# Kernel tuning notes

Hardware: AMD Instinct MI355X
Metric: run time of the kernel (lower is better)

Reference implementation:

```python
import jax, jax.numpy as jnp
import numpy as np

HEADS = 8
EMBED = 64  # out_channels per head
N_OP = 100000
N_MC = 20000
N_EDGE = 300000
EPS = 1e-16  # matches PyG softmax denominator epsilon


def hetero_gat(x_src, x_dst, edge_index, W, att, n_dst):
    """GAT conv: gather -> per-edge score -> segment softmax over dst -> scatter-sum -> head mean.
    x_src: [Ns, F], x_dst: [Nd, F], edge_index: [2, E] (row0=src, row1=dst),
    W: [HEADS*EMBED, F], att: [1, HEADS, 2*EMBED].
    """
    hs = (x_src @ W.T).reshape(-1, HEADS, EMBED)  # [Ns,H,C]
    hd = (x_dst @ W.T).reshape(-1, HEADS, EMBED)  # [Nd,H,C]
    src, dst = edge_index[0], edge_index[1]
    x_j = hs[src]                                  # [E,H,C] (source/neighbor)
    x_i = hd[dst]                                  # [E,H,C] (destination)
    att_i = att[0, :, :EMBED]                      # [H,C] weights for x_i part of concat
    att_j = att[0, :, EMBED:]                      # [H,C] weights for x_j part
    # (cat([x_i,x_j],-1) * att).sum(-1) without materializing the concat
    alpha = jnp.einsum('ehc,hc->eh', x_i, att_i) + jnp.einsum('ehc,hc->eh', x_j, att_j)
    # segment softmax grouped by destination node
    m = jax.ops.segment_max(alpha, dst, num_segments=n_dst)  # [Nd,H]
    e = jnp.exp(alpha - m[dst])
    s = jax.ops.segment_sum(e, dst, num_segments=n_dst)      # [Nd,H]
    alpha = e / (s[dst] + EPS)                                # [E,H]
    msg = x_j * alpha[..., None]                              # [E,H,C]
    out = jax.ops.segment_sum(msg, dst, num_segments=n_dst)   # [Nd,H,C]
    return out.mean(axis=1)                                   # [Nd,C] multi-head mean


def setup_inputs() -> dict:
    key = jax.random.key(0)
    ks = jax.random.split(key, 12)
    op_nodes = jax.random.normal(ks[0], (N_OP, 4), dtype=jnp.float32)
    mc_nodes = jax.random.normal(ks[1], (N_MC, 2), dtype=jnp.float32)
    src = jax.random.randint(ks[2], (N_EDGE,), 0, N_OP)
    dst = jax.random.randint(ks[3], (N_EDGE,), 0, N_MC)
    edge_index_om = jnp.stack([src, dst]).astype(jnp.int64)
    g = 0.1
    params = {
        'W_op': jax.random.normal(ks[4], (EMBED, 4), dtype=jnp.float32) * g,
        'b_op': jnp.zeros((EMBED,), dtype=jnp.float32),
        'W_mc': jax.random.normal(ks[5], (EMBED, 2), dtype=jnp.float32) * g,
        'b_mc': jnp.zeros((EMBED,), dtype=jnp.float32),
        'W_om': jax.random.normal(ks[6], (HEADS * EMBED, EMBED), dtype=jnp.float32) * g,
        'att_om': jax.random.normal(ks[7], (1, HEADS, 2 * EMBED), dtype=jnp.float32) * g,
        'W_mo': jax.random.normal(ks[8], (HEADS * EMBED, EMBED), dtype=jnp.float32) * g,
        'att_mo': jax.random.normal(ks[9], (1, HEADS, 2 * EMBED), dtype=jnp.float32) * g,
    }
    return {'op_nodes': op_nodes, 'mc_nodes': mc_nodes, 'edge_index_om': edge_index_om, **params}


def reference(op_nodes, mc_nodes, edge_index_om, W_op, b_op, W_mc, b_mc,
              W_om, att_om, W_mo, att_mo):
    h_op = jax.nn.elu(op_nodes @ W_op.T + b_op)   # [N_OP, 64]
    h_mc = jax.nn.elu(mc_nodes @ W_mc.T + b_mc)   # [N_MC, 64]
    # op -> mc
    h_mc_new = hetero_gat(h_op, h_mc, edge_index_om, W_om, att_om, N_MC)
    h_mc = jax.nn.elu(h_mc + h_mc_new)
    # mc -> op (reversed edges)
    edge_index_mo = jnp.stack([edge_index_om[1], edge_index_om[0]])
    h_op_new = hetero_gat(h_mc, h_op, edge_index_mo, W_mo, att_mo, N_OP)
    h_op = jax.nn.elu(h_op + h_op_new)
    return (h_op, h_mc)
```

## Files before the change

kernel.cpp:

```cpp
#include <hip/hip_runtime.h>
#include <hip/hip_bf16.h>

using bf16 = __hip_bfloat16;
typedef __attribute__((ext_vector_type(8))) short short8;
typedef __attribute__((ext_vector_type(4))) float f32x4;

__device__ __forceinline__ unsigned short f2bf(float f) {
  bf16 h = __float2bfloat16(f);
  return *reinterpret_cast<unsigned short*>(&h);
}
__device__ __forceinline__ float bf2f(unsigned short u) {
  return __uint_as_float(((unsigned)u) << 16);
}

__device__ __forceinline__ float loadf(const void* p, int i, int is_f32) {
  if (is_f32) return ((const float*)p)[i];
  return __bfloat162float(((const bf16*)p)[i]);
}

__global__ __launch_bounds__(256) void init_kernel(
    const int* __restrict__ ei, const unsigned short* __restrict__ x,
    int* __restrict__ flags, int* __restrict__ cnt1, int n1,
    int* __restrict__ cnt2, int n2) {
  int t = threadIdx.x;
  int g = blockIdx.x * 256 + t;
  int stride = gridDim.x * 256;
  for (int i = g; i < n1; i += stride) cnt1[i] = 0;
  for (int i = g; i < n2; i += stride) cnt2[i] = 0;
  if (blockIdx.x == 0) {
    __shared__ int red[256];
    int o = 0, big = 0;
    for (int i = t; i < 2048; i += 256) {
      o |= ei[2 * i + 1];
      float v = __uint_as_float(((unsigned)x[2 * i]) << 16);
      if (!(fabsf(v) < 1000.f)) big = 1;
    }
    red[t] = o;
    __syncthreads();
    for (int d = 128; d > 0; d >>= 1) {
      if (t < d) red[t] |= red[t + d];
      __syncthreads();
    }
    int o_all = red[0];
    __syncthreads();
    red[t] = big;
    __syncthreads();
    for (int d = 128; d > 0; d >>= 1) {
      if (t < d) red[t] |= red[t + d];
      __syncthreads();
    }
    if (t == 0) {
      flags[0] = red[0];
      flags[1] = (o_all == 0) ? 1 : 0;
    }
  }
}

__device__ __forceinline__ int edge_src(const int* ei, int E, int e, int i64) {
  return i64 ? ei[2 * e] : ei[e];
}
__device__ __forceinline__ int edge_dst(const int* ei, int E, int e, int i64) {
  return i64 ? ei[2 * E + 2 * e] : ei[E + e];
}

template <int FIN>
__device__ __forceinline__ void node_body4(
    const void* x, const void* W, const void* b, int is_f32,
    const float* vj, bf16* h_out, unsigned short* ea_out, int n0, int N) {
  int lane = threadIdx.x & 63;
  float wreg[FIN];
#pragma unroll
  for (int f = 0; f < FIN; ++f) wreg[f] = loadf(W, lane * FIN + f, is_f32);
  float bias = loadf(b, lane, is_f32);
  float vjreg[8];
  if (ea_out) {
#pragma unroll
    for (int h = 0; h < 8; ++h) vjreg[h] = vj[h * 64 + lane];
  }
#pragma unroll
  for (int j = 0; j < 4; ++j) {
    int n = n0 + j;
    if (n >= N) break;
    float acc = bias;
#pragma unroll
    for (int f = 0; f < FIN; ++f)
      acc += loadf(x, n * FIN + f, is_f32) * wreg[f];
    float hv = acc > 0.f ? acc : expm1f(acc);
    h_out[(unsigned)(n << 6) + lane] = __float2bfloat16(hv);
    if (ea_out) {
      float p[8];
#pragma unroll
      for (int h = 0; h < 8; ++h) p[h] = hv * vjreg[h];
#pragma unroll
      for (int i = 0; i < 4; ++i) {
        float send = (lane & 4) ? p[i] : p[i + 4];
        float keep = (lane & 4) ? p[i + 4] : p[i];
        p[i] = keep + __shfl_xor(send, 4, 64);
      }
#pragma unroll
      for (int i = 0; i < 2; ++i) {
        float send = (lane & 2) ? p[i] : p[i + 2];
        float keep = (lane & 2) ? p[i + 2] : p[i];
        p[i] = keep + __shfl_xor(send, 2, 64);
      }
      {
        float send = (lane & 1) ? p[0] : p[1];
        float keep = (lane & 1) ? p[1] : p[0];
        p[0] = keep + __shfl_xor(send, 1, 64);
      }
      p[0] += __shfl_xor(p[0], 8, 64);
      p[0] += __shfl_xor(p[0], 16, 64);
      p[0] += __shfl_xor(p[0], 32, 64);
      if (lane < 8) ea_out[(unsigned)(n << 3) + lane] = f2bf(__expf(p[0]));
    }
  }
}

__global__ __launch_bounds__(256) void front_kernel(
    const void* __restrict__ x_op, const void* __restrict__ W_op,
    const void* __restrict__ b_op, const void* __restrict__ x_mc,
    const void* __restrict__ W_mc, const void* __restrict__ b_mc,
    const void* __restrict__ W1, const void* __restrict__ att1,
    const void* __restrict__ W2, const void* __restrict__ att2,
    const int* __restrict__ ei, const int* __restrict__ flags,
    float* __restrict__ vj1, bf16* __restrict__ Wrt1, float* __restrict__ vj2,
    bf16* __restrict__ Wrt2, bf16* __restrict__ h_op,
    unsigned short* __restrict__ ea_op, bf16* __restrict__ h_mc,
    int* __restrict__ cnt_dst, int* __restrict__ cnt_src, int n_op, int n_mc,
    int E, int nbo, int nbm) {
  int bid = blockIdx.x;
  int is_f32 = flags[0];
  if (bid < nbo) {
    int n0 = bid * 16 + (threadIdx.x >> 6) * 4;
    if (n0 < n_op)
      node_body4<4>(x_op, W_op, b_op, is_f32, vj1, h_op, ea_op, n0, n_op);
  } else if (bid < nbo + nbm) {
    int n0 = (bid - nbo) * 16 + (threadIdx.x >> 6) * 4;
    if (n0 < n_mc)
      node_body4<2>(x_mc, W_mc, b_mc, is_f32, nullptr, h_mc, nullptr, n0, n_mc);
  } else if (bid < nbo + nbm + 256) {
    int pb = bid - nbo - nbm;
    int side = pb >= 128;
    const void* W = side ? W2 : W1;
    const void* att = side ? att2 : att1;
    float* vj = side ? vj2 : vj1;
    bf16* Wrt = side ? Wrt2 : Wrt1;
    int tt = (pb & 127) * 256 + threadIdx.x;
    if (tt < 32768) {
      int c = tt >> 9, k = tt & 511;
      int f = k >> 3, h = k & 7;
      Wrt[tt] = __float2bfloat16(loadf(W, ((h << 6) + c) * 64 + f, is_f32));
    }
    if (tt < 512) {
      int hh = tt >> 6, ff = tt & 63;
      float s = 0.f;
      for (int cc = 0; cc < 64; ++cc)
        s += loadf(att, hh * 128 + 64 + cc, is_f32) *
             loadf(W, ((hh << 6) + cc) * 64 + ff, is_f32);
      vj[tt] = s;
    }
  } else {
    int i64 = flags[1];
    int e = (bid - nbo - nbm - 256) * 256 + threadIdx.x;
    if (e < E) {
      atomicAdd(&cnt_dst[edge_dst(ei, E, e, i64)], 1);
      atomicAdd(&cnt_src[edge_src(ei, E, e, i64)], 1);
    }
  }
}

__global__ __launch_bounds__(256) void scan_bsum2(
    const int* __restrict__ cnt1, int n1, int nb1, const int* __restrict__ cnt2,
    int n2, int* __restrict__ bsum1, int* __restrict__ bsum2) {
  __shared__ int red[256];
  int t = threadIdx.x;
  int side = (int)blockIdx.x >= nb1;
  const int* cnt = side ? cnt2 : cnt1;
  int n = side ? n2 : n1;
  int blk = side ? (blockIdx.x - nb1) : blockIdx.x;
  int base = blk * 2048 + t * 8;
  int s = 0;
#pragma unroll
  for (int i = 0; i < 8; ++i)
    if (base + i < n) s += cnt[base + i];
  red[t] = s;
  __syncthreads();
  for (int d = 128; d > 0; d >>= 1) {
    if (t < d) red[t] += red[t + d];
    __syncthreads();
  }
  if (t == 0) (side ? bsum2 : bsum1)[blk] = red[0];
}

__global__ __launch_bounds__(256) void scan_write2(
    const int* __restrict__ cnt1, int n1, int nb1,
    const int* __restrict__ bsum1, int* __restrict__ offs1,
    int* __restrict__ cur1, const int* __restrict__ cnt2, int n2, int nb2,
    const int* __restrict__ bsum2, int* __restrict__ offs2,
    int* __restrict__ cur2) {
  __shared__ int red[256];
  __shared__ int base_s;
  int t = threadIdx.x;
  int side = (int)blockIdx.x >= nb1;
  const int* cnt = side ? cnt2 : cnt1;
  const int* bsum = side ? bsum2 : bsum1;
  int* offs = side ? offs2 : offs1;
  int* cur = side ? cur2 : cur1;
  int n = side ? n2 : n1;
  int nb = side ? nb2 : nb1;
  int blk = side ? (blockIdx.x - nb1) : blockIdx.x;
  if (t == 0) {
    int b = 0;
    for (int i = 0; i < blk; ++i) b += bsum[i];
    base_s = b;
  }
  int base = blk * 2048 + t * 8;
  int c[8];
  int s = 0;
#pragma unroll
  for (int i = 0; i < 8; ++i) {
    c[i] = (base + i < n) ? cnt[base + i] : 0;
    s += c[i];
  }
  red[t] = s;
  __syncthreads();
  for (int d = 1; d < 256; d <<= 1) {
    int v = red[t];
    int add = (t >= d) ? red[t - d] : 0;
    __syncthreads();
    red[t] = v + add;
    __syncthreads();
  }
  int run = base_s + red[t] - s;
#pragma unroll
  for (int i = 0; i < 8; ++i) {
    if (base + i < n) {
      offs[base + i] = run;
      cur[base + i] = run;
      run += c[i];
    }
  }
  if (blk == nb - 1 && t == 255) offs[n] = base_s + red[255];
}

__global__ __launch_bounds__(256) void fill_edges(
    const int* __restrict__ ei, int E, const int* __restrict__ flags,
    int* __restrict__ cur1, int* __restrict__ srcs1, int* __restrict__ cur2,
    int* __restrict__ srcs2) {
  int i64 = flags[1];
  int e = blockIdx.x * blockDim.x + threadIdx.x;
  if (e < E) {
    int s = edge_src(ei, E, e, i64), d = edge_dst(ei, E, e, i64);
    int p = atomicAdd(&cur1[d], 1);
    srcs1[p] = s;
    int q = atomicAdd(&cur2[s], 1);
    srcs2[q] = d;
  }
}

template <bool WRITE_AJ, bool WRITE_BF>
__global__ __launch_bounds__(256) void gat_fused(
    int Nd, const int* __restrict__ offs, const int* __restrict__ srcs,
    const unsigned short* __restrict__ ea, const bf16* __restrict__ h_src,
    const bf16* __restrict__ Wrt, const bf16* __restrict__ h_res,
    float* __restrict__ out_f32, bf16* __restrict__ out_bf,
    const float* __restrict__ vj_next, unsigned short* __restrict__ ea_next) {
  __shared__ __align__(16) unsigned short Zl[16 * 520];
  __shared__ float ajp[4][16][8];

  int t = threadIdx.x;
  int wv = t >> 6, lane = t & 63;
  int d0 = blockIdx.x * 16;
  int sj = lane >> 4;
  int fq = lane & 15;

  int dlo = d0 + wv * 4;
  int wo0 = offs[min(dlo + 0, Nd)];
  int wo1 = offs[min(dlo + 1, Nd)];
  int wo2 = offs[min(dlo + 2, Nd)];
  int wo3 = offs[min(dlo + 3, Nd)];
  int wo4 = offs[min(dlo + 4, Nd)];
  int woj = sj == 0 ? wo0 : sj == 1 ? wo1 : sj == 2 ? wo2 : wo3;
  int woj1 = sj == 0 ? wo1 : sj == 1 ? wo2 : sj == 2 ? wo3 : wo4;
  int nj = woj1 - woj;

  float z[8][4];
#pragma unroll
  for (int h = 0; h < 8; ++h)
#pragma unroll
    for (int f = 0; f < 4; ++f) z[h][f] = 0.f;
  float s8[8];
#pragma unroll
  for (int h = 0; h < 8; ++h) s8[h] = 0.f;

  const unsigned short* hsrc_u = (const unsigned short*)h_src;

  int rmax = max(nj, __shfl_xor(nj, 16, 64));
  rmax = max(rmax, __shfl_xor(rmax, 32, 64));

  for (int r0 = 0; r0 < rmax; r0 += 4) {
    unsigned srcq[4];
#pragma unroll
    for (int q = 0; q < 4; ++q) {
      int r = r0 + q;
      srcq[q] = (r < nj) ? (unsigned)srcs[woj + r] : 0u;
    }
    ushort4 uq[4];
    short8 eq[4];
#pragma unroll
    for (int q = 0; q < 4; ++q) {
      unsigned s = srcq[q];
      uq[q] = *(const ushort4*)(hsrc_u + (s << 6) + (fq << 2));
      eq[q] = *(const short8*)(ea + (s << 3));
    }
#pragma unroll
    for (int q = 0; q < 4; ++q) {
      bool act = (r0 + q) < nj;
      float w[8];
#pragma unroll
      for (int h = 0; h < 8; ++h)
        w[h] = act ? bf2f((unsigned short)eq[q][h]) : 0.f;
      float x0 = bf2f(uq[q].x), x1 = bf2f(uq[q].y);
      float x2 = bf2f(uq[q].z), x3 = bf2f(uq[q].w);
#pragma unroll
      for (int h = 0; h < 8; ++h) {
        z[h][0] += w[h] * x0;
        z[h][1] += w[h] * x1;
        z[h][2] += w[h] * x2;
        z[h][3] += w[h] * x3;
        s8[h] += w[h];
      }
    }
  }

  float si[8];
#pragma unroll
  for (int h = 0; h < 8; ++h) si[h] = s8[h] > 0.f ? 1.f / s8[h] : 0.f;
  int row = wv * 4 + sj;
#pragma unroll
  for (int fi = 0; fi < 4; ++fi) {
    int4 pk;
    pk.x = ((int)f2bf(z[1][fi] * si[1]) << 16) | f2bf(z[0][fi] * si[0]);
    pk.y = ((int)f2bf(z[3][fi] * si[3]) << 16) | f2bf(z[2][fi] * si[2]);
    pk.z = ((int)f2bf(z[5][fi] * si[5]) << 16) | f2bf(z[4][fi] * si[4]);
    pk.w = ((int)f2bf(z[7][fi] * si[7]) << 16) | f2bf(z[6][fi] * si[6]);
    *(int4*)&Zl[row * 520 + (fq * 4 + fi) * 8] = pk;
  }

  int arow = lane & 15;
  int kg = lane >> 4;
  int col = wv * 16 + arow;
  float res[4];
#pragma unroll
  for (int r = 0; r < 4; ++r) {
    int d = d0 + kg * 4 + r;
    res[r] =
        (d < Nd) ? __bfloat162float(h_res[(unsigned)(d << 6) + col]) : 0.f;
  }
  __syncthreads();

  f32x4 acc = {0.f, 0.f, 0.f, 0.f};
#pragma unroll
  for (int kt = 0; kt < 16; ++kt) {
    int kbase = kt * 32 + kg * 8;
    short8 a = *(const short8*)&Zl[arow * 520 + kbase];
    short8 b = *(const short8*)&Wrt[(unsigned)((wv * 16 + arow) * 512 + kbase)];
    acc = __builtin_amdgcn_mfma_f32_16x16x32_bf16(a, b, acc, 0, 0, 0);
  }

  float o_r[4];
#pragma unroll
  for (int r = 0; r < 4; ++r) {
    int d = d0 + kg * 4 + r;
    float o = 0.f;
    if (d < Nd) {
      float v = res[r] + 0.125f * acc[r];
      o = v > 0.f ? v : expm1f(v);
      out_f32[(unsigned)(d << 6) + col] = o;
      if (WRITE_BF) out_bf[(unsigned)(d << 6) + col] = __float2bfloat16(o);
    }
    o_r[r] = o;
  }

  if (WRITE_AJ) {
#pragma unroll
    for (int r = 0; r < 4; ++r) {
      int dloc = kg * 4 + r;
      float p[8];
#pragma unroll
      for (int h = 0; h < 8; ++h) p[h] = o_r[r] * vj_next[h * 64 + col];
#pragma unroll
      for (int i = 0; i < 4; ++i) {
        float send = (arow & 4) ? p[i] : p[i + 4];
        float keep = (arow & 4) ? p[i + 4] : p[i];
        p[i] = keep + __shfl_xor(send, 4, 64);
      }
#pragma unroll
      for (int i = 0; i < 2; ++i) {
        float send = (arow & 2) ? p[i] : p[i + 2];
        float keep = (arow & 2) ? p[i + 2] : p[i];
        p[i] = keep + __shfl_xor(send, 2, 64);
      }
      {
        float send = (arow & 1) ? p[0] : p[1];
        float keep = (arow & 1) ? p[1] : p[0];
        p[0] = keep + __shfl_xor(send, 1, 64);
      }
      p[0] += __shfl_xor(p[0], 8, 64);
      if (arow < 8) ajp[wv][dloc][arow] = p[0];
    }
    __syncthreads();
    if (t < 128) {
      int dloc = t >> 3, h = t & 7;
      int d = d0 + dloc;
      if (d < Nd) {
        float s = ajp[0][dloc][h] + ajp[1][dloc][h] + ajp[2][dloc][h] +
                  ajp[3][dloc][h];
        ea_next[(unsigned)(d << 3) + h] = f2bf(__expf(s));
      }
    }
  }
}

extern "C" void kernel_launch(void* const* d_in, const int* in_sizes, int n_in,
                              void* d_out, int out_size, void* d_ws,
                              size_t ws_size, hipStream_t stream) {
  const void* op_nodes = d_in[0];
  const void* mc_nodes = d_in[1];
  const int* ei        = (const int*)d_in[2];
  const void* W_op     = d_in[3];
  const void* b_op     = d_in[4];
  const void* W_mc     = d_in[5];
  const void* b_mc     = d_in[6];
  const void* W_om     = d_in[7];
  const void* att_om   = d_in[8];
  const void* W_mo     = d_in[9];
  const void* att_mo   = d_in[10];

  int n_op = in_sizes[0] / 4;
  int n_mc = in_sizes[1] / 2;
  int E    = in_sizes[2] / 2;

  char* ws = (char*)d_ws;
  size_t off = 0;
  auto alloc = [&](size_t bytes) -> void* {
    void* p = ws + off;
    off = (off + bytes + 255) & ~(size_t)255;
    return p;
  };
  int* flags   = (int*)alloc(16);
  bf16* h_op   = (bf16*)alloc((size_t)n_op * 64 * 2);
  bf16* h_mc   = (bf16*)alloc((size_t)n_mc * 64 * 2);
  bf16* h_mc2  = (bf16*)alloc((size_t)n_mc * 64 * 2);
  unsigned short* ea_op = (unsigned short*)alloc((size_t)n_op * 8 * 2);
  unsigned short* ea_mc = (unsigned short*)alloc((size_t)n_mc * 8 * 2);
  float* vj_om = (float*)alloc(512 * 4);
  float* vj_mo = (float*)alloc(512 * 4);
  bf16* Wrt_om = (bf16*)alloc(32768 * 2);
  bf16* Wrt_mo = (bf16*)alloc(32768 * 2);
  int* cnt1  = (int*)alloc((size_t)n_mc * 4);
  int* cnt2  = (int*)alloc((size_t)n_op * 4);
  int* offs1 = (int*)alloc((size_t)(n_mc + 1) * 4);
  int* cur1  = (int*)alloc((size_t)n_mc * 4);
  int* srcs1 = (int*)alloc((size_t)E * 4);
  int* offs2 = (int*)alloc((size_t)(n_op + 1) * 4);
  int* cur2  = (int*)alloc((size_t)n_op * 4);
  int* srcs2 = (int*)alloc((size_t)E * 4);
  int* bsum1 = (int*)alloc(256 * 4);
  int* bsum2 = (int*)alloc(256 * 4);

  float* out_op = (float*)d_out;
  float* out_mc = out_op + (size_t)n_op * 64;

  init_kernel<<<512, 256, 0, stream>>>(ei, (const unsigned short*)op_nodes,
                                       flags, cnt1, n_mc, cnt2, n_op);

  int nbo = (n_op + 15) / 16, nbm = (n_mc + 15) / 16;
  int nbe = (E + 255) / 256;
  front_kernel<<<nbo + nbm + 256 + nbe, 256, 0, stream>>>(
      op_nodes, W_op, b_op, mc_nodes, W_mc, b_mc, W_om, att_om, W_mo, att_mo,
      ei, flags, vj_om, Wrt_om, vj_mo, Wrt_mo, h_op, ea_op, h_mc, cnt1, cnt2,
      n_op, n_mc, E, nbo, nbm);

  int nb1 = (n_mc + 2047) / 2048, nb2 = (n_op + 2047) / 2048;
  scan_bsum2<<<nb1 + nb2, 256, 0, stream>>>(cnt1, n_mc, nb1, cnt2, n_op, bsum1,
                                            bsum2);
  scan_write2<<<nb1 + nb2, 256, 0, stream>>>(cnt1, n_mc, nb1, bsum1, offs1,
                                             cur1, cnt2, n_op, nb2, bsum2,
                                             offs2, cur2);
  fill_edges<<<nbe, 256, 0, stream>>>(ei, E, flags, cur1, srcs1, cur2, srcs2);

  gat_fused<true, true><<<(n_mc + 15) / 16, 256, 0, stream>>>(
      n_mc, offs1, srcs1, ea_op, h_op, Wrt_om, h_mc, out_mc, h_mc2, vj_mo,
      ea_mc);
  gat_fused<false, false><<<(n_op + 15) / 16, 256, 0, stream>>>(
      n_op, offs2, srcs2, ea_mc, h_mc2, Wrt_mo, h_op, out_op, (bf16*)nullptr,
      (const float*)nullptr, (unsigned short*)nullptr);
}
```

Before: 207.6 us.

## Aggregate neighbor messages with MFMA over block-wide edge chunks

Replaces the per-lane scalar FMA aggregation of weighted source features with a block-cooperative scheme. Each 32-edge chunk of the block's CSR range is staged into shared memory: features are transposed, and attention weights and per-edge destination slots are recorded. The weighted segment-sum then runs as masked bf16 MFMAs, with a one-hot destination mask applied to the weights. This aims to remove the heavy per-thread FMA work and the load imbalance across destinations within a wavefront, at the cost of extra syncthreads, LDS staging and bf16 rounding of the masked weights.

```diff
diff --git a/kernel.cpp b/kernel.cpp
--- a/kernel.cpp
+++ b/kernel.cpp
@@ -267,88 +267,129 @@
     const float* __restrict__ vj_next, unsigned short* __restrict__ ea_next) {
   __shared__ __align__(16) unsigned short Zl[16 * 520];
   __shared__ float ajp[4][16][8];
+  __shared__ __align__(16) unsigned short XsT[64 * 40];
+  __shared__ __align__(16) unsigned short esT[8 * 40];
+  __shared__ __align__(8) unsigned char dsb[32];
+  __shared__ int bnd[17];
+  __shared__ float silds[4][16][2];
 
   int t = threadIdx.x;
   int wv = t >> 6, lane = t & 63;
-  int d0 = blockIdx.x * 16;
-  int sj = lane >> 4;
-  int fq = lane & 15;
-
-  int dlo = d0 + wv * 4;
-  int wo0 = offs[min(dlo + 0, Nd)];
-  int wo1 = offs[min(dlo + 1, Nd)];
-  int wo2 = offs[min(dlo + 2, Nd)];
-  int wo3 = offs[min(dlo + 3, Nd)];
-  int wo4 = offs[min(dlo + 4, Nd)];
-  int woj = sj == 0 ? wo0 : sj == 1 ? wo1 : sj == 2 ? wo2 : wo3;
-  int woj1 = sj == 0 ? wo1 : sj == 1 ? wo2 : sj == 2 ? wo3 : wo4;
-  int nj = woj1 - woj;
-
-  float z[8][4];
-#pragma unroll
-  for (int h = 0; h < 8; ++h)
-#pragma unroll
-    for (int f = 0; f < 4; ++f) z[h][f] = 0.f;
-  float s8[8];
-#pragma unroll
-  for (int h = 0; h < 8; ++h) s8[h] = 0.f;
-
-  const unsigned short* hsrc_u = (const unsigned short*)h_src;
-
-  int rmax = max(nj, __shfl_xor(nj, 16, 64));
-  rmax = max(rmax, __shfl_xor(rmax, 32, 64));
-
-  for (int r0 = 0; r0 < rmax; r0 += 4) {
-    unsigned srcq[4];
-#pragma unroll
-    for (int q = 0; q < 4; ++q) {
-      int r = r0 + q;
-      srcq[q] = (r < nj) ? (unsigned)srcs[woj + r] : 0u;
-    }
-    ushort4 uq[4];
-    short8 eq[4];
-#pragma unroll
-    for (int q = 0; q < 4; ++q) {
-      unsigned s = srcq[q];
-      uq[q] = *(const ushort4*)(hsrc_u + (s << 6) + (fq << 2));
-      eq[q] = *(const short8*)(ea + (s << 3));
-    }
-#pragma unroll
-    for (int q = 0; q < 4; ++q) {
-      bool act = (r0 + q) < nj;
-      float w[8];
-#pragma unroll
-      for (int h = 0; h < 8; ++h)
-        w[h] = act ? bf2f((unsigned short)eq[q][h]) : 0.f;
-      float x0 = bf2f(uq[q].x), x1 = bf2f(uq[q].y);
-      float x2 = bf2f(uq[q].z), x3 = bf2f(uq[q].w);
-#pragma unroll
-      for (int h = 0; h < 8; ++h) {
-        z[h][0] += w[h] * x0;
-        z[h][1] += w[h] * x1;
-        z[h][2] += w[h] * x2;
-        z[h][3] += w[h] * x3;
-        s8[h] += w[h];
-      }
-    }
-  }
-
-  float si[8];
-#pragma unroll
-  for (int h = 0; h < 8; ++h) si[h] = s8[h] > 0.f ? 1.f / s8[h] : 0.f;
-  int row = wv * 4 + sj;
-#pragma unroll
-  for (int fi = 0; fi < 4; ++fi) {
-    int4 pk;
-    pk.x = ((int)f2bf(z[1][fi] * si[1]) << 16) | f2bf(z[0][fi] * si[0]);
-    pk.y = ((int)f2bf(z[3][fi] * si[3]) << 16) | f2bf(z[2][fi] * si[2]);
-    pk.z = ((int)f2bf(z[5][fi] * si[5]) << 16) | f2bf(z[4][fi] * si[4]);
-    pk.w = ((int)f2bf(z[7][fi] * si[7]) << 16) | f2bf(z[6][fi] * si[6]);
-    *(int4*)&Zl[row * 520 + (fq * 4 + fi) * 8] = pk;
-  }
-
   int arow = lane & 15;
   int kg = lane >> 4;
+  int d0 = blockIdx.x * 16;
+  int h0 = wv * 2;
+
+  if (t < 17) bnd[t] = offs[min(d0 + t, Nd)];
+
+  f32x4 acc[2][4];
+#pragma unroll
+  for (int h = 0; h < 2; ++h)
+#pragma unroll
+    for (int c = 0; c < 4; ++c) acc[h][c] = (f32x4){0.f, 0.f, 0.f, 0.f};
+  float sp0 = 0.f, sp1 = 0.f;
+
+  __syncthreads();
+  int beg = bnd[0];
+  int nE = bnd[16] - beg;
+
+  const unsigned short* hsrc_u = (const unsigned short*)h_src;
+
+  for (int cb = 0; cb < nE; cb += 32) {
+    int cn = min(32, nE - cb);
+    if (t < 32) {
+      int e = t;
+      bool v = e < cn;
+      int ge = beg + cb + e;
+      int j = 255;
+      if (v) {
+        j = 0;
+        if (ge >= bnd[j + 8]) j += 8;
+        if (ge >= bnd[j + 4]) j += 4;
+        if (ge >= bnd[j + 2]) j += 2;
+        if (ge >= bnd[j + 1]) j += 1;
+      }
+      dsb[e] = (unsigned char)j;
+      if (v) {
+        unsigned sidx = (unsigned)srcs[ge];
+        short8 eav = *(const short8*)(ea + (sidx << 3));
+#pragma unroll
+        for (int h = 0; h < 8; ++h)
+          esT[h * 40 + e] = (unsigned short)eav[h];
+      }
+    }
+    {
+      int e = t >> 3, fg = t & 7;
+      if (e < cn) {
+        unsigned sidx = (unsigned)srcs[beg + cb + e];
+        short8 xv = *(const short8*)(hsrc_u + (sidx << 6) + (fg << 3));
+        int eb = ((((e >> 3) + (fg & 3)) & 3) << 3) + (e & 7);
+#pragma unroll
+        for (int i = 0; i < 8; ++i)
+          XsT[(fg * 8 + i) * 40 + eb] = (unsigned short)xv[i];
+      }
+    }
+    __syncthreads();
+    int2 dsw = *(const int2*)&dsb[kg * 8];
+    int m16[4];
+#pragma unroll
+    for (int jj = 0; jj < 4; ++jj) {
+      int w32 = (jj < 2) ? dsw.x : dsw.y;
+      int b0 = (w32 >> ((jj & 1) * 16)) & 255;
+      int b1 = (w32 >> ((jj & 1) * 16 + 8)) & 255;
+      m16[jj] = ((b0 == arow) ? 0x0000FFFF : 0) | ((b1 == arow) ? 0xFFFF0000 : 0);
+    }
+    short8 bfr[4];
+#pragma unroll
+    for (int c = 0; c < 4; ++c) {
+      int f = c * 16 + arow;
+      int blk = (kg + ((f >> 3) & 3)) & 3;
+      bfr[c] = *(const short8*)&XsT[f * 40 + (blk << 3)];
+    }
+#pragma unroll
+    for (int h = 0; h < 2; ++h) {
+      int4 es4 = *(const int4*)&esT[(h0 + h) * 40 + (kg << 3)];
+      int4 aw;
+      aw.x = es4.x & m16[0];
+      aw.y = es4.y & m16[1];
+      aw.z = es4.z & m16[2];
+      aw.w = es4.w & m16[3];
+      float ssum =
+          bf2f((unsigned short)(aw.x & 0xFFFF)) + bf2f((unsigned short)((unsigned)aw.x >> 16)) +
+          bf2f((unsigned short)(aw.y & 0xFFFF)) + bf2f((unsigned short)((unsigned)aw.y >> 16)) +
+          bf2f((unsigned short)(aw.z & 0xFFFF)) + bf2f((unsigned short)((unsigned)aw.z >> 16)) +
+          bf2f((unsigned short)(aw.w & 0xFFFF)) + bf2f((unsigned short)((unsigned)aw.w >> 16));
+      if (h == 0) sp0 += ssum; else sp1 += ssum;
+      short8 af = *(short8*)&aw;
+#pragma unroll
+      for (int c = 0; c < 4; ++c)
+        acc[h][c] =
+            __builtin_amdgcn_mfma_f32_16x16x32_bf16(af, bfr[c], acc[h][c], 0, 0, 0);
+    }
+    __syncthreads();
+  }
+
+  sp0 += __shfl_xor(sp0, 16, 64);
+  sp0 += __shfl_xor(sp0, 32, 64);
+  sp1 += __shfl_xor(sp1, 16, 64);
+  sp1 += __shfl_xor(sp1, 32, 64);
+  if (lane < 16) {
+    silds[wv][lane][0] = sp0 > 0.f ? 1.f / sp0 : 0.f;
+    silds[wv][lane][1] = sp1 > 0.f ? 1.f / sp1 : 0.f;
+  }
+#pragma unroll
+  for (int r = 0; r < 4; ++r) {
+    int dstslot = kg * 4 + r;
+    float si0 = silds[wv][dstslot][0];
+    float si1 = silds[wv][dstslot][1];
+#pragma unroll
+    for (int c = 0; c < 4; ++c) {
+      int kp = (c * 16 + arow) * 8 + h0;
+      Zl[dstslot * 520 + kp + 0] = f2bf(acc[0][c][r] * si0);
+      Zl[dstslot * 520 + kp + 1] = f2bf(acc[1][c][r] * si1);
+    }
+  }
+
   int col = wv * 16 + arow;
   float res[4];
 #pragma unroll
@@ -359,13 +400,13 @@
   }
   __syncthreads();
 
-  f32x4 acc = {0.f, 0.f, 0.f, 0.f};
+  f32x4 eacc = {0.f, 0.f, 0.f, 0.f};
 #pragma unroll
   for (int kt = 0; kt < 16; ++kt) {
     int kbase = kt * 32 + kg * 8;
     short8 a = *(const short8*)&Zl[arow * 520 + kbase];
     short8 b = *(const short8*)&Wrt[(unsigned)((wv * 16 + arow) * 512 + kbase)];
-    acc = __builtin_amdgcn_mfma_f32_16x16x32_bf16(a, b, acc, 0, 0, 0);
+    eacc = __builtin_amdgcn_mfma_f32_16x16x32_bf16(a, b, eacc, 0, 0, 0);
   }
 
   float o_r[4];
@@ -374,7 +415,7 @@
     int d = d0 + kg * 4 + r;
     float o = 0.f;
     if (d < Nd) {
-      float v = res[r] + 0.125f * acc[r];
+      float v = res[r] + 0.125f * eacc[r];
       o = v > 0.f ? v : expm1f(v);
       out_f32[(unsigned)(d << 6) + col] = o;
       if (WRITE_BF) out_bf[(unsigned)(d << 6) + col] = __float2bfloat16(o);
```

After: 226.2 us. +9.0%, slower.
